# Performance work log

Hardware: AMD Instinct MI355X
Metric: run time of the kernel (lower is better)

## Reference

```python
import jax, jax.numpy as jnp
import numpy as np

B, N, GN, GS = 16, 100000, 4096, 64  # batch, points, num_groups, group_size


def setup_inputs() -> dict:
    key = jax.random.key(0)
    k1, k2, k3 = jax.random.split(key, 3)
    x_proto = jax.random.normal(k1, (B, N, 3), dtype=jnp.float32)
    template = jax.random.normal(k2, (N, 3), dtype=jnp.float32)
    groups = jax.random.randint(k3, (GN, GS), 0, N, dtype=jnp.int32)
    return {"x_proto": x_proto, "template": template, "groups": groups}


def reference(x_proto, template, groups):
    # x_proto: [B, N, 3], template: [N, 3], groups: [GN, GS] int indices
    b, n, _ = x_proto.shape
    Yg = template[groups]                      # [GN, GS, 3] gathered template
    Xg = x_proto[:, groups]                    # [B, GN, GS, 3] gathered current points

    # Kabsch: align template group Y to current X (R @ Y + t ~ X)
    muY = Yg.mean(axis=1)                      # [GN, 3]
    muX = Xg.mean(axis=2)                      # [B, GN, 3]
    Yc = Yg - muY[:, None, :]
    Xc = Xg - muX[:, :, None, :]
    H = jnp.einsum('gni,bgnj->bgij', Yc, Xc)   # [B, GN, 3, 3] covariance
    U, S, Vh = jnp.linalg.svd(H)
    V = jnp.swapaxes(Vh, -2, -1)
    R0 = V @ jnp.swapaxes(U, -2, -1)
    det = jnp.linalg.det(R0)                   # [B, GN]
    # flip last column of V where det < 0 to get a proper rotation
    s = jnp.where(det < 0, -1.0, 1.0).astype(x_proto.dtype)
    col_scale = jnp.stack([jnp.ones_like(s), jnp.ones_like(s), s], axis=-1)  # [B, GN, 3]
    R = (V * col_scale[..., None, :]) @ jnp.swapaxes(U, -2, -1)              # [B, GN, 3, 3]
    t = muX - jnp.einsum('bgij,gj->bgi', R, muY)                             # [B, GN, 3]

    # project template group through (R, t)
    Xg_proj = jnp.einsum('bgij,gnj->bgni', R, Yg) + t[:, :, None, :]         # [B, GN, GS, 3]

    # scatter-add with overlap counting, then average
    flat_idx = groups.reshape(-1)              # [GN*GS]
    out = jnp.zeros_like(x_proto).at[:, flat_idx].add(Xg_proj.reshape(b, -1, 3))
    counts = jnp.zeros((n,), dtype=x_proto.dtype).at[flat_idx].add(1.0)
    counts = jnp.maximum(counts, 1.0)
    return out / counts[None, :, None]
```

## Files before the change

### kernel.cpp

```cpp
#include <hip/hip_runtime.h>
#include <math.h>

static constexpr int BB = 16;
static constexpr int NN = 100000;
static constexpr int GN = 4096;
static constexpr int GS = 64;
static constexpr int NP = BB * GN;
static constexpr int NE = GN * GS;
static constexpr int NBLK = (NN + 255) / 256;

__device__ __forceinline__ float wsum64(float v) {
#pragma unroll
  for (int off = 32; off > 0; off >>= 1) v += __shfl_xor(v, off, 64);
  return v;
}

__global__ __launch_bounds__(256) void k_xpad(
    const float4* __restrict__ x, const float4* __restrict__ tpl,
    float4* __restrict__ x4, float4* __restrict__ tpl4,
    int4* __restrict__ cnt4, int* __restrict__ gtotal) {
  int t = blockIdx.x * 256 + threadIdx.x;
  if (t == 0) *gtotal = 0;
  if (t < NN / 4) {
    cnt4[t] = make_int4(0, 0, 0, 0);
    float4 a = tpl[t * 3 + 0], b = tpl[t * 3 + 1], c = tpl[t * 3 + 2];
    tpl4[t * 4 + 0] = make_float4(a.x, a.y, a.z, 0.f);
    tpl4[t * 4 + 1] = make_float4(a.w, b.x, b.y, 0.f);
    tpl4[t * 4 + 2] = make_float4(b.z, b.w, c.x, 0.f);
    tpl4[t * 4 + 3] = make_float4(c.y, c.z, c.w, 0.f);
  }
  if (t >= BB * NN / 4) return;
  float4 a = x[t * 3 + 0], b = x[t * 3 + 1], c = x[t * 3 + 2];
  x4[t * 4 + 0] = make_float4(a.x, a.y, a.z, 0.f);
  x4[t * 4 + 1] = make_float4(a.w, b.x, b.y, 0.f);
  x4[t * 4 + 2] = make_float4(b.z, b.w, c.x, 0.f);
  x4[t * 4 + 3] = make_float4(c.y, c.z, c.w, 0.f);
}

__global__ __launch_bounds__(256) void k_tpl(
    const float4* __restrict__ tpl4, const int* __restrict__ groups,
    float* __restrict__ Yg, float* __restrict__ GmY, int* __restrict__ cnt) {
  int g    = blockIdx.x * 4 + (threadIdx.x >> 6);
  int lane = threadIdx.x & 63;
  int idx = groups[g * GS + lane];
  atomicAdd(&cnt[idx], 1);
  float4 y = tpl4[idx];
  float* o = Yg + ((size_t)g * GS + lane) * 3;
  o[0] = y.x; o[1] = y.y; o[2] = y.z;
  float sy0 = wsum64(y.x), sy1 = wsum64(y.y), sy2 = wsum64(y.z);
  if (lane == 0) {
    const float inv = 1.0f / 64.0f;
    *(float4*)(GmY + (size_t)g * 4) =
        make_float4(sy0 * inv, sy1 * inv, sy2 * inv, 0.0f);
  }
}

__global__ __launch_bounds__(256) void k_stats(
    const float4* __restrict__ x4, const float* __restrict__ Yg,
    const float* __restrict__ GmY, const int* __restrict__ groups,
    float* __restrict__ Ht) {
  int bid  = (blockIdx.x & 7) * 512 + (blockIdx.x >> 3);
  int wid4 = bid * 4 + (threadIdx.x >> 6);
  int lane = threadIdx.x & 63;
  int s    = lane >> 4;
  int l4   = lane & 15;
  int p = wid4 * 4 + s;
  int b = p >> 12;
  int g = p & (GN - 1);

  int4 iv = *(const int4*)(groups + (size_t)g * GS + l4 * 4);
  const float4* yv = (const float4*)(Yg + ((size_t)g * GS + l4 * 4) * 3);
  float4 ya = yv[0], yb = yv[1], yc = yv[2];

  const float4* xb4 = x4 + (size_t)b * NN;
  float sx0 = 0.f, sx1 = 0.f, sx2 = 0.f;
  float h00 = 0.f, h01 = 0.f, h02 = 0.f;
  float h10 = 0.f, h11 = 0.f, h12 = 0.f;
  float h20 = 0.f, h21 = 0.f, h22 = 0.f;

#define ACC(Y0, Y1, Y2, IDX)                                   \
  {                                                            \
    float4 xv = xb4[IDX];                                      \
    sx0 += xv.x; sx1 += xv.y; sx2 += xv.z;                     \
    h00 += (Y0) * xv.x; h01 += (Y0) * xv.y; h02 += (Y0) * xv.z;\
    h10 += (Y1) * xv.x; h11 += (Y1) * xv.y; h12 += (Y1) * xv.z;\
    h20 += (Y2) * xv.x; h21 += (Y2) * xv.y; h22 += (Y2) * xv.z;\
  }
  ACC(ya.x, ya.y, ya.z, iv.x);
  ACC(ya.w, yb.x, yb.y, iv.y);
  ACC(yb.z, yb.w, yc.x, iv.z);
  ACC(yc.y, yc.z, yc.w, iv.w);
#undef ACC

#define RED(V)                                                 \
  V += __shfl_xor(V, 8, 64); V += __shfl_xor(V, 4, 64);        \
  V += __shfl_xor(V, 2, 64); V += __shfl_xor(V, 1, 64);
  RED(sx0) RED(sx1) RED(sx2)
  RED(h00) RED(h01) RED(h02)
  RED(h10) RED(h11) RED(h12)
  RED(h20) RED(h21) RED(h22)
#undef RED

  if (l4 == 0) {
    const float inv = 1.0f / 64.0f;
    float4 m = *(const float4*)(GmY + (size_t)g * 4);
    float mx0 = sx0 * inv, mx1 = sx1 * inv, mx2 = sx2 * inv;
    float4 o0 = make_float4(mx0, mx1, mx2, h00 - m.x * sx0);
    float4 o1 = make_float4(h01 - m.x * sx1, h02 - m.x * sx2,
                            h10 - m.y * sx0, h11 - m.y * sx1);
    float4 o2 = make_float4(h12 - m.y * sx2, h20 - m.z * sx0,
                            h21 - m.z * sx1, h22 - m.z * sx2);
    float* o = Ht + (size_t)p * 12;
    *(float4*)(o + 0) = o0;
    *(float4*)(o + 4) = o1;
    *(float4*)(o + 8) = o2;
  }
}

#define JROT(P, Q, RR)                                                        \
  {                                                                           \
    float apq = K[P][Q];                                                      \
    if (fabsf(apq) > 1e-30f) {                                                \
      float app = K[P][P], aqq = K[Q][Q];                                     \
      float tau = (aqq - app) / (2.0f * apq);                                 \
      float tt = copysignf(1.0f, tau) / (fabsf(tau) + sqrtf(1.0f + tau*tau)); \
      float cc = 1.0f / sqrtf(1.0f + tt * tt);                                \
      float ss = tt * cc;                                                     \
      K[P][P] = app - tt * apq;                                               \
      K[Q][Q] = aqq + tt * apq;                                               \
      K[P][Q] = 0.0f; K[Q][P] = 0.0f;                                         \
      float krp = K[RR][P], krq = K[RR][Q];                                   \
      K[RR][P] = cc * krp - ss * krq; K[P][RR] = K[RR][P];                    \
      K[RR][Q] = ss * krp + cc * krq; K[Q][RR] = K[RR][Q];                    \
      float v0p = V[0][P], v0q = V[0][Q];                                     \
      float v1p = V[1][P], v1q = V[1][Q];                                     \
      float v2p = V[2][P], v2q = V[2][Q];                                     \
      V[0][P] = cc * v0p - ss * v0q; V[0][Q] = ss * v0p + cc * v0q;           \
      V[1][P] = cc * v1p - ss * v1q; V[1][Q] = ss * v1p + cc * v1q;           \
      V[2][P] = cc * v2p - ss * v2q; V[2][Q] = ss * v2p + cc * v2q;           \
    }                                                                         \
  }

#define FIN(AA, BBi, CC)                                                      \
  {                                                                           \
    float va0 = V[0][AA], va1 = V[1][AA], va2 = V[2][AA];                     \
    float vb0 = V[0][BBi], vb1 = V[1][BBi], vb2 = V[2][BBi];                  \
    float vc0 = V[0][CC], vc1 = V[1][CC], vc2 = V[2][CC];                     \
    float ua0 = A[0][0]*va0 + A[0][1]*va1 + A[0][2]*va2;                      \
    float ua1 = A[1][0]*va0 + A[1][1]*va1 + A[1][2]*va2;                      \
    float ua2 = A[2][0]*va0 + A[2][1]*va1 + A[2][2]*va2;                      \
    float il = 1.0f / sqrtf(ua0*ua0 + ua1*ua1 + ua2*ua2 + 1e-30f);            \
    ua0 *= il; ua1 *= il; ua2 *= il;                                          \
    float ub0 = A[0][0]*vb0 + A[0][1]*vb1 + A[0][2]*vb2;                      \
    float ub1 = A[1][0]*vb0 + A[1][1]*vb1 + A[1][2]*vb2;                      \
    float ub2 = A[2][0]*vb0 + A[2][1]*vb1 + A[2][2]*vb2;                      \
    il = 1.0f / sqrtf(ub0*ub0 + ub1*ub1 + ub2*ub2 + 1e-30f);                  \
    ub0 *= il; ub1 *= il; ub2 *= il;                                          \
    float dd = ua0*ub0 + ua1*ub1 + ua2*ub2;                                   \
    ub0 -= dd * ua0; ub1 -= dd * ua1; ub2 -= dd * ua2;                        \
    il = 1.0f / sqrtf(ub0*ub0 + ub1*ub1 + ub2*ub2 + 1e-30f);                  \
    ub0 *= il; ub1 *= il; ub2 *= il;                                          \
    float uc0 = ua1*ub2 - ua2*ub1;                                            \
    float uc1 = ua2*ub0 - ua0*ub2;                                            \
    float uc2 = ua0*ub1 - ua1*ub0;                                            \
    R[0][0] = va0*ua0 + vb0*ub0 + dsg*vc0*uc0;                                \
    R[0][1] = va0*ua1 + vb0*ub1 + dsg*vc0*uc1;                                \
    R[0][2] = va0*ua2 + vb0*ub2 + dsg*vc0*uc2;                                \
    R[1][0] = va1*ua0 + vb1*ub0 + dsg*vc1*uc0;                                \
    R[1][1] = va1*ua1 + vb1*ub1 + dsg*vc1*uc1;                                \
    R[1][2] = va1*ua2 + vb1*ub2 + dsg*vc1*uc2;                                \
    R[2][0] = va2*ua0 + vb2*ub0 + dsg*vc2*uc0;                                \
    R[2][1] = va2*ua1 + vb2*ub1 + dsg*vc2*uc1;                                \
    R[2][2] = va2*ua2 + vb2*ub2 + dsg*vc2*uc2;                                \
  }

__global__ __launch_bounds__(256) void k_svd(
    const float* __restrict__ Ht, const float* __restrict__ GmY,
    float* __restrict__ Qt) {
  int p = blockIdx.x * 256 + threadIdx.x;
  if (p >= NP) return;
  int g = p & (GN - 1);
  const float* h = Ht + (size_t)p * 12;
  float4 f0 = *(const float4*)(h + 0);
  float4 f1 = *(const float4*)(h + 4);
  float4 f2 = *(const float4*)(h + 8);
  float4 m  = *(const float4*)(GmY + (size_t)g * 4);
  float mx0 = f0.x, mx1 = f0.y, mx2 = f0.z;
  float my0 = m.x, my1 = m.y, my2 = m.z;
  float A[3][3];
  A[0][0] = f0.w; A[0][1] = f1.x; A[0][2] = f1.y;
  A[1][0] = f1.z; A[1][1] = f1.w; A[1][2] = f2.x;
  A[2][0] = f2.y; A[2][1] = f2.z; A[2][2] = f2.w;

  float K[3][3];
#pragma unroll
  for (int i = 0; i < 3; ++i)
#pragma unroll
    for (int j = 0; j < 3; ++j)
      K[i][j] = A[0][i]*A[0][j] + A[1][i]*A[1][j] + A[2][i]*A[2][j];

  float V[3][3] = {{1.f,0.f,0.f},{0.f,1.f,0.f},{0.f,0.f,1.f}};
#pragma unroll
  for (int sweep = 0; sweep < 5; ++sweep) {
    JROT(0, 1, 2);
    JROT(0, 2, 1);
    JROT(1, 2, 0);
  }

  float d0 = K[0][0], d1 = K[1][1], d2 = K[2][2];
  float detV = V[0][0]*(V[1][1]*V[2][2] - V[1][2]*V[2][1])
             - V[0][1]*(V[1][0]*V[2][2] - V[1][2]*V[2][0])
             + V[0][2]*(V[1][0]*V[2][1] - V[1][1]*V[2][0]);
  float dsg = (detV < 0.0f) ? -1.0f : 1.0f;

  float R[3][3];
  if (d0 <= d1 && d0 <= d2) {
    FIN(1, 2, 0);
  } else if (d1 <= d0 && d1 <= d2) {
    FIN(2, 0, 1);
  } else {
    FIN(0, 1, 2);
  }

  float t0 = mx0 - (R[0][0]*my0 + R[0][1]*my1 + R[0][2]*my2);
  float t1 = mx1 - (R[1][0]*my0 + R[1][1]*my1 + R[1][2]*my2);
  float t2 = mx2 - (R[2][0]*my0 + R[2][1]*my1 + R[2][2]*my2);

  float qw, qx, qy, qz;
  float tr = R[0][0] + R[1][1] + R[2][2];
  if (tr > 0.f) {
    float S = sqrtf(tr + 1.0f) * 2.0f;
    qw = 0.25f * S;
    qx = (R[2][1] - R[1][2]) / S;
    qy = (R[0][2] - R[2][0]) / S;
    qz = (R[1][0] - R[0][1]) / S;
  } else if (R[0][0] > R[1][1] && R[0][0] > R[2][2]) {
    float S = sqrtf(1.0f + R[0][0] - R[1][1] - R[2][2]) * 2.0f;
    qw = (R[2][1] - R[1][2]) / S;
    qx = 0.25f * S;
    qy = (R[0][1] + R[1][0]) / S;
    qz = (R[0][2] + R[2][0]) / S;
  } else if (R[1][1] > R[2][2]) {
    float S = sqrtf(1.0f + R[1][1] - R[0][0] - R[2][2]) * 2.0f;
    qw = (R[0][2] - R[2][0]) / S;
    qx = (R[0][1] + R[1][0]) / S;
    qy = 0.25f * S;
    qz = (R[1][2] + R[2][1]) / S;
  } else {
    float S = sqrtf(1.0f + R[2][2] - R[0][0] - R[1][1]) * 2.0f;
    qw = (R[1][0] - R[0][1]) / S;
    qx = (R[0][2] + R[2][0]) / S;
    qy = (R[1][2] + R[2][1]) / S;
    qz = 0.25f * S;
  }
  float il2 = 1.0f / sqrtf(qw*qw + qx*qx + qy*qy + qz*qz);
  qw *= il2; qx *= il2; qy *= il2; qz *= il2;

  float* o = Qt + (size_t)p * 8;
  *(float4*)(o + 0) = make_float4(qx, qy, qz, qw);
  *(float4*)(o + 4) = make_float4(t0, t1, t2, 0.f);
}

__global__ __launch_bounds__(256) void k_alloc(
    const int* __restrict__ cnt, int* __restrict__ gtotal,
    int2* __restrict__ rs_cnt, int* __restrict__ cursor) {
  int t = blockIdx.x * 256 + threadIdx.x;
  int lane = threadIdx.x & 63;
  int v = (t < NN) ? cnt[t] : 0;
  int sc = v;
#pragma unroll
  for (int off = 1; off < 64; off <<= 1) {
    int u = __shfl_up(sc, off, 64);
    if (lane >= off) sc += u;
  }
  int wtotal = __shfl(sc, 63, 64);
  int base = 0;
  if (lane == 63) base = atomicAdd(gtotal, wtotal);
  base = __shfl(base, 63, 64);
  if (t < NN) {
    rs_cnt[t] = make_int2(base + sc - v, v);
    cursor[t] = 0;
  }
}

__global__ __launch_bounds__(256) void k_fill(
    const int* __restrict__ groups, const int2* __restrict__ rs_cnt,
    int* __restrict__ cursor, int* __restrict__ entries) {
  int e = blockIdx.x * 256 + threadIdx.x;
  if (e >= NE) return;
  int n = groups[e];
  int pos = atomicAdd(&cursor[n], 1);
  entries[rs_cnt[n].x + pos] = e >> 6;
}

__global__ __launch_bounds__(256) void k_gather(
    const float4* __restrict__ tpl4, const int2* __restrict__ rs_cnt,
    const int* __restrict__ entries, const float* __restrict__ Qt,
    float* __restrict__ out) {
  int nl = threadIdx.x >> 4;
  int b  = threadIdx.x & 15;
  int n  = blockIdx.x * 16 + nl;
  if (n >= NN) return;
  int2 rc = rs_cnt[n];
  int s = rc.x, c = rc.y;
  float4 y = tpl4[n];
  float p0 = 0.f, p1 = 0.f, p2 = 0.f;
  const float* Qb = Qt + (size_t)b * GN * 8;
  for (int j = 0; j < c; ++j) {
    int g = entries[s + j];
    const float* qt = Qb + (size_t)g * 8;
    float4 q = *(const float4*)(qt + 0);
    float4 tv = *(const float4*)(qt + 4);
    float tx = 2.f * (q.y * y.z - q.z * y.y);
    float ty = 2.f * (q.z * y.x - q.x * y.z);
    float tz = 2.f * (q.x * y.y - q.y * y.x);
    p0 += y.x + q.w * tx + (q.y * tz - q.z * ty) + tv.x;
    p1 += y.y + q.w * ty + (q.z * tx - q.x * tz) + tv.y;
    p2 += y.z + q.w * tz + (q.x * ty - q.y * tx) + tv.z;
  }
  float inv = 1.0f / fmaxf((float)c, 1.0f);
  float* o = out + ((size_t)b * NN + (size_t)n) * 3;
  *(float3*)o = make_float3(p0 * inv, p1 * inv, p2 * inv);
}

extern "C" void kernel_launch(void* const* d_in, const int* in_sizes, int n_in,
                              void* d_out, int out_size, void* d_ws, size_t ws_size,
                              hipStream_t stream) {
  const float* x      = (const float*)d_in[0];
  const float* tpl    = (const float*)d_in[1];
  const int*   groups = (const int*)d_in[2];
  float* out = (float*)d_out;

  char* ws = (char*)d_ws;
  size_t o_x4   = 0;
  size_t o_tpl4 = o_x4 + 25600000;
  size_t o_yg   = o_tpl4 + 1600000;
  size_t o_ht   = o_yg + 3145728;
  size_t o_qt   = o_ht + 3145728;
  size_t o_gmy  = o_qt + 2097152;
  size_t o_cnt  = o_gmy + 65536;
  size_t o_rsc  = o_cnt + 400000;
  size_t o_cur  = o_rsc + 800000;
  size_t o_gt   = o_cur + 400000;
  size_t o_ent  = o_gt + 64;
  float* x4     = (float*)(ws + o_x4);
  float* tpl4   = (float*)(ws + o_tpl4);
  float* Yg     = (float*)(ws + o_yg);
  float* Ht     = (float*)(ws + o_ht);
  float* Qt     = (float*)(ws + o_qt);
  float* GmY    = (float*)(ws + o_gmy);
  int*   cnt    = (int*)(ws + o_cnt);
  int2*  rs_cnt = (int2*)(ws + o_rsc);
  int*   cursor = (int*)(ws + o_cur);
  int*   gtotal = (int*)(ws + o_gt);
  int*   entries= (int*)(ws + o_ent);

  k_xpad<<<(BB * NN / 4 + 255) / 256, 256, 0, stream>>>(
      (const float4*)x, (const float4*)tpl, (float4*)x4, (float4*)tpl4,
      (int4*)cnt, gtotal);
  k_tpl<<<GN / 4, 256, 0, stream>>>((const float4*)tpl4, groups, Yg, GmY, cnt);
  k_stats<<<NP / 16, 256, 0, stream>>>((const float4*)x4, Yg, GmY, groups, Ht);
  k_svd<<<NP / 256, 256, 0, stream>>>(Ht, GmY, Qt);
  k_alloc<<<NBLK, 256, 0, stream>>>(cnt, gtotal, rs_cnt, cursor);
  k_fill<<<NE / 256, 256, 0, stream>>>(groups, rs_cnt, cursor, entries);
  k_gather<<<(NN + 15) / 16, 256, 0, stream>>>(
      (const float4*)tpl4, rs_cnt, entries, Qt, out);
}
```

Before: 134.8 us.

## Split gather into per-entry projection and CSR-ordered reduction

Replaces the per-point gather kernel with two stages. k_proj computes each group entry's projected point for all 16 batches and writes it into a CSR-sorted buffer. k_reduce then sums each point's contiguous slots and divides by the count. This removes the indirect per-point reads of group rotation data in the old gather, which were uncoalesced. The cost is an extra intermediate buffer of about 50 MB (B*NE*3 floats) that is written and read back, plus scattered 12-byte writes from k_proj. The CSR build kernels are also moved ahead of the SVD kernel in the launch order.

Measured after the change: 179.5 us. +33.1%, slower.

```diff
diff --git a/kernel.cpp b/kernel.cpp
--- a/kernel.cpp
+++ b/kernel.cpp
@@ -285,40 +285,54 @@
 
 __global__ __launch_bounds__(256) void k_fill(
     const int* __restrict__ groups, const int2* __restrict__ rs_cnt,
-    int* __restrict__ cursor, int* __restrict__ entries) {
+    int* __restrict__ cursor, int* __restrict__ eslot) {
   int e = blockIdx.x * 256 + threadIdx.x;
   if (e >= NE) return;
   int n = groups[e];
   int pos = atomicAdd(&cursor[n], 1);
-  entries[rs_cnt[n].x + pos] = e >> 6;
-}
-
-__global__ __launch_bounds__(256) void k_gather(
-    const float4* __restrict__ tpl4, const int2* __restrict__ rs_cnt,
-    const int* __restrict__ entries, const float* __restrict__ Qt,
-    float* __restrict__ out) {
-  int nl = threadIdx.x >> 4;
-  int b  = threadIdx.x & 15;
-  int n  = blockIdx.x * 16 + nl;
-  if (n >= NN) return;
-  int2 rc = rs_cnt[n];
-  int s = rc.x, c = rc.y;
+  eslot[e] = rs_cnt[n].x + pos;
+}
+
+__global__ __launch_bounds__(256) void k_proj(
+    const int* __restrict__ groups, const int* __restrict__ eslot,
+    const float4* __restrict__ tpl4, const float* __restrict__ Qt,
+    float* __restrict__ proj) {
+  int e = blockIdx.x * 256 + threadIdx.x;
+  int g = e >> 6;
+  int n = groups[e];
+  int slot = eslot[e];
   float4 y = tpl4[n];
-  float p0 = 0.f, p1 = 0.f, p2 = 0.f;
-  const float* Qb = Qt + (size_t)b * GN * 8;
-  for (int j = 0; j < c; ++j) {
-    int g = entries[s + j];
-    const float* qt = Qb + (size_t)g * 8;
-    float4 q = *(const float4*)(qt + 0);
+#pragma unroll 4
+  for (int b = 0; b < BB; ++b) {
+    const float* qt = Qt + ((size_t)b * GN + g) * 8;
+    float4 q  = *(const float4*)(qt + 0);
     float4 tv = *(const float4*)(qt + 4);
     float tx = 2.f * (q.y * y.z - q.z * y.y);
     float ty = 2.f * (q.z * y.x - q.x * y.z);
     float tz = 2.f * (q.x * y.y - q.y * y.x);
-    p0 += y.x + q.w * tx + (q.y * tz - q.z * ty) + tv.x;
-    p1 += y.y + q.w * ty + (q.z * tx - q.x * tz) + tv.y;
-    p2 += y.z + q.w * tz + (q.x * ty - q.y * tx) + tv.z;
-  }
-  float inv = 1.0f / fmaxf((float)c, 1.0f);
+    float p0 = y.x + q.w * tx + (q.y * tz - q.z * ty) + tv.x;
+    float p1 = y.y + q.w * ty + (q.z * tx - q.x * tz) + tv.y;
+    float p2 = y.z + q.w * tz + (q.x * ty - q.y * tx) + tv.z;
+    float* o = proj + ((size_t)b * NE + (size_t)slot) * 3;
+    o[0] = p0; o[1] = p1; o[2] = p2;
+  }
+}
+
+__global__ __launch_bounds__(256) void k_reduce(
+    const int2* __restrict__ rs_cnt, const float* __restrict__ proj,
+    float* __restrict__ out) {
+  int n = blockIdx.x * 256 + threadIdx.x;
+  if (n >= NN) return;
+  int b = blockIdx.y;
+  int2 rc = rs_cnt[n];
+  const float* pp = proj + ((size_t)b * NE + (size_t)rc.x) * 3;
+  float p0 = 0.f, p1 = 0.f, p2 = 0.f;
+  for (int j = 0; j < rc.y; ++j) {
+    p0 += pp[j * 3 + 0];
+    p1 += pp[j * 3 + 1];
+    p2 += pp[j * 3 + 2];
+  }
+  float inv = 1.0f / fmaxf((float)rc.y, 1.0f);
   float* o = out + ((size_t)b * NN + (size_t)n) * 3;
   *(float3*)o = make_float3(p0 * inv, p1 * inv, p2 * inv);
 }
@@ -342,7 +356,8 @@
   size_t o_rsc  = o_cnt + 400000;
   size_t o_cur  = o_rsc + 800000;
   size_t o_gt   = o_cur + 400000;
-  size_t o_ent  = o_gt + 64;
+  size_t o_esl  = o_gt + 64;
+  size_t o_proj = o_esl + 1048576;
   float* x4     = (float*)(ws + o_x4);
   float* tpl4   = (float*)(ws + o_tpl4);
   float* Yg     = (float*)(ws + o_yg);
@@ -353,16 +368,17 @@
   int2*  rs_cnt = (int2*)(ws + o_rsc);
   int*   cursor = (int*)(ws + o_cur);
   int*   gtotal = (int*)(ws + o_gt);
-  int*   entries= (int*)(ws + o_ent);
+  int*   eslot  = (int*)(ws + o_esl);
+  float* proj   = (float*)(ws + o_proj);
 
   k_xpad<<<(BB * NN / 4 + 255) / 256, 256, 0, stream>>>(
       (const float4*)x, (const float4*)tpl, (float4*)x4, (float4*)tpl4,
       (int4*)cnt, gtotal);
   k_tpl<<<GN / 4, 256, 0, stream>>>((const float4*)tpl4, groups, Yg, GmY, cnt);
   k_stats<<<NP / 16, 256, 0, stream>>>((const float4*)x4, Yg, GmY, groups, Ht);
+  k_alloc<<<NBLK, 256, 0, stream>>>(cnt, gtotal, rs_cnt, cursor);
+  k_fill<<<NE / 256, 256, 0, stream>>>(groups, rs_cnt, cursor, eslot);
   k_svd<<<NP / 256, 256, 0, stream>>>(Ht, GmY, Qt);
-  k_alloc<<<NBLK, 256, 0, stream>>>(cnt, gtotal, rs_cnt, cursor);
-  k_fill<<<NE / 256, 256, 0, stream>>>(groups, rs_cnt, cursor, entries);
-  k_gather<<<(NN + 15) / 16, 256, 0, stream>>>(
-      (const float4*)tpl4, rs_cnt, entries, Qt, out);
-}
+  k_proj<<<NE / 256, 256, 0, stream>>>(groups, eslot, (const float4*)tpl4, Qt, proj);
+  k_reduce<<<dim3(NBLK, BB), 256, 0, stream>>>(rs_cnt, proj, out);
+}
```

## Pad per-point entry lists to 4 and remap gather to one thread per point

Applied to the files above, without the earlier changes.

Each point's range in the scatter-inverse entry list is padded to a multiple of four, and the padding slots are zero-filled. This lets the gather kernel read entries as int4 and issue four quaternion/translation loads per iteration, with weight masking for the padding. The gather grid is remapped so each thread handles one point for a fixed batch index, taken from blockIdx.y, which makes the output stores contiguous. The alloc and fill kernels are also moved before the SVD kernel. The padding adds extra entry storage and wasted loads, and threads in a wave now have divergent loop trip counts.

Result: slower. 141.5 us (+5.0%).

```diff
diff --git a/kernel.cpp b/kernel.cpp
--- a/kernel.cpp
+++ b/kernel.cpp
@@ -263,11 +263,13 @@
 
 __global__ __launch_bounds__(256) void k_alloc(
     const int* __restrict__ cnt, int* __restrict__ gtotal,
-    int2* __restrict__ rs_cnt, int* __restrict__ cursor) {
+    int2* __restrict__ rs_cnt, int* __restrict__ cursor,
+    int* __restrict__ entries) {
   int t = blockIdx.x * 256 + threadIdx.x;
   int lane = threadIdx.x & 63;
-  int v = (t < NN) ? cnt[t] : 0;
-  int sc = v;
+  int v  = (t < NN) ? cnt[t] : 0;
+  int vp = (v + 3) & ~3;
+  int sc = vp;
 #pragma unroll
   for (int off = 1; off < 64; off <<= 1) {
     int u = __shfl_up(sc, off, 64);
@@ -278,8 +280,10 @@
   if (lane == 63) base = atomicAdd(gtotal, wtotal);
   base = __shfl(base, 63, 64);
   if (t < NN) {
-    rs_cnt[t] = make_int2(base + sc - v, v);
+    int s = base + sc - vp;
+    rs_cnt[t] = make_int2(s, v);
     cursor[t] = 0;
+    for (int k = v; k < vp; ++k) entries[s + k] = 0;
   }
 }
 
@@ -297,26 +301,44 @@
     const float4* __restrict__ tpl4, const int2* __restrict__ rs_cnt,
     const int* __restrict__ entries, const float* __restrict__ Qt,
     float* __restrict__ out) {
-  int nl = threadIdx.x >> 4;
-  int b  = threadIdx.x & 15;
-  int n  = blockIdx.x * 16 + nl;
+  int n = blockIdx.x * 256 + threadIdx.x;
   if (n >= NN) return;
+  int b = blockIdx.y;
   int2 rc = rs_cnt[n];
   int s = rc.x, c = rc.y;
   float4 y = tpl4[n];
   float p0 = 0.f, p1 = 0.f, p2 = 0.f;
   const float* Qb = Qt + (size_t)b * GN * 8;
-  for (int j = 0; j < c; ++j) {
-    int g = entries[s + j];
-    const float* qt = Qb + (size_t)g * 8;
-    float4 q = *(const float4*)(qt + 0);
-    float4 tv = *(const float4*)(qt + 4);
-    float tx = 2.f * (q.y * y.z - q.z * y.y);
-    float ty = 2.f * (q.z * y.x - q.x * y.z);
-    float tz = 2.f * (q.x * y.y - q.y * y.x);
-    p0 += y.x + q.w * tx + (q.y * tz - q.z * ty) + tv.x;
-    p1 += y.y + q.w * ty + (q.z * tx - q.x * tz) + tv.y;
-    p2 += y.z + q.w * tz + (q.x * ty - q.y * tx) + tv.z;
+
+  for (int j = 0; j < c; j += 4) {
+    int4 ev = *(const int4*)(entries + s + j);
+    const float* qp0 = Qb + (size_t)ev.x * 8;
+    const float* qp1 = Qb + (size_t)ev.y * 8;
+    const float* qp2 = Qb + (size_t)ev.z * 8;
+    const float* qp3 = Qb + (size_t)ev.w * 8;
+    float4 qa = *(const float4*)(qp0);
+    float4 ta = *(const float4*)(qp0 + 4);
+    float4 qb = *(const float4*)(qp1);
+    float4 tb = *(const float4*)(qp1 + 4);
+    float4 qc = *(const float4*)(qp2);
+    float4 tc = *(const float4*)(qp2 + 4);
+    float4 qd = *(const float4*)(qp3);
+    float4 td = *(const float4*)(qp3 + 4);
+#define QACC(Q, T, K)                                                   \
+    {                                                                   \
+      float w = (j + (K) < c) ? 1.f : 0.f;                              \
+      float tx = 2.f * ((Q).y * y.z - (Q).z * y.y);                     \
+      float ty = 2.f * ((Q).z * y.x - (Q).x * y.z);                     \
+      float tz = 2.f * ((Q).x * y.y - (Q).y * y.x);                     \
+      p0 += w * (y.x + (Q).w * tx + ((Q).y * tz - (Q).z * ty) + (T).x); \
+      p1 += w * (y.y + (Q).w * ty + ((Q).z * tx - (Q).x * tz) + (T).y); \
+      p2 += w * (y.z + (Q).w * tz + ((Q).x * ty - (Q).y * tx) + (T).z); \
+    }
+    QACC(qa, ta, 0)
+    QACC(qb, tb, 1)
+    QACC(qc, tc, 2)
+    QACC(qd, td, 3)
+#undef QACC
   }
   float inv = 1.0f / fmaxf((float)c, 1.0f);
   float* o = out + ((size_t)b * NN + (size_t)n) * 3;
@@ -360,9 +382,9 @@
       (int4*)cnt, gtotal);
   k_tpl<<<GN / 4, 256, 0, stream>>>((const float4*)tpl4, groups, Yg, GmY, cnt);
   k_stats<<<NP / 16, 256, 0, stream>>>((const float4*)x4, Yg, GmY, groups, Ht);
+  k_alloc<<<NBLK, 256, 0, stream>>>(cnt, gtotal, rs_cnt, cursor, entries);
+  k_fill<<<NE / 256, 256, 0, stream>>>(groups, rs_cnt, cursor, entries);
   k_svd<<<NP / 256, 256, 0, stream>>>(Ht, GmY, Qt);
-  k_alloc<<<NBLK, 256, 0, stream>>>(cnt, gtotal, rs_cnt, cursor);
-  k_fill<<<NE / 256, 256, 0, stream>>>(groups, rs_cnt, cursor, entries);
-  k_gather<<<(NN + 15) / 16, 256, 0, stream>>>(
+  k_gather<<<dim3(NBLK, BB), 256, 0, stream>>>(
       (const float4*)tpl4, rs_cnt, entries, Qt, out);
 }
```
